# Performance work log

Hardware: AMD Instinct MI355X
Metric: run time of the kernel (lower is better)

The kernel has to match this reference:

```python
import jax, jax.numpy as jnp
import numpy as np

N_HEAD = 16

def setup_inputs() -> dict:
    key = jax.random.key(0)
    k1, k2, k3 = jax.random.split(key, 3)
    B, T, D = 2, 2048, 1024
    x = jax.random.normal(k1, (B, T, D), dtype=jnp.float32)
    sigma_qkv = float(np.sqrt(2.0 / (D + 3 * D)))
    sigma_out = float(np.sqrt(2.0 / (D + D)))
    W_qkv = jax.random.truncated_normal(k2, -3.0, 3.0, (3 * D, D), dtype=jnp.float32) * sigma_qkv
    W_out = jax.random.truncated_normal(k3, -3.0, 3.0, (D, D), dtype=jnp.float32) * sigma_out
    return {"x": x, "W_qkv": W_qkv, "W_out": W_out}


def reference(x, W_qkv, W_out):
    B, T, C = x.shape
    H = N_HEAD
    hd = C // H
    qkv = x @ W_qkv.T  # (B,T,3C)
    q, k, v = jnp.split(qkv, 3, axis=-1)
    # (B,T,C) -> (B,H,T,hd)
    q = q.reshape(B, T, H, hd).transpose(0, 2, 1, 3)
    k = k.reshape(B, T, H, hd).transpose(0, 2, 1, 3)
    v = v.reshape(B, T, H, hd).transpose(0, 2, 1, 3)
    scale = 1.0 / jnp.sqrt(jnp.asarray(hd, dtype=x.dtype))
    score = jnp.einsum('bhqd,bhkd->bhqk', q, k) * scale  # (B,H,T,T)
    causal = jnp.tril(jnp.ones((T, T), dtype=bool))
    score = jnp.where(causal, score, -jnp.inf)
    attn = jax.nn.softmax(score, axis=-1)
    out = jnp.einsum('bhqk,bhkd->bhqd', attn, v)  # (B,H,T,hd)
    out = out.transpose(0, 2, 1, 3).reshape(B, T, C)
    return out @ W_out.T
```

## Files before the change

kernel.cpp:

```cpp
#include <hip/hip_runtime.h>
#include <hip/hip_bf16.h>
#include <cstdint>

typedef unsigned short u16;
typedef __attribute__((ext_vector_type(8))) short bf16x8;
typedef __attribute__((ext_vector_type(4))) float f32x4;

#define T_SEQ 2048
#define NHEAD 16
#define HDIM  64
#define NB    2

__device__ __forceinline__ float bf2f(uint32_t h) { return __uint_as_float(h << 16); }
__device__ __forceinline__ u16 f2bf(float f) {
    uint32_t u = __float_as_uint(f);
    u += 0x7fffu + ((u >> 16) & 1u);
    return (u16)(u >> 16);
}

__device__ __forceinline__ void gl_lds16(const u16* g, u16* s) {
    __builtin_amdgcn_global_load_lds(
        (const __attribute__((address_space(1))) unsigned int*)g,
        (__attribute__((address_space(3))) unsigned int*)s, 16, 0, 0);
}

__global__ void detect_dtype(const uint32_t* __restrict__ x, int* __restrict__ flag) {
    __shared__ int red[4];
    int c = 0;
#pragma unroll
    for (int j = 0; j < 4; j++) {
        uint32_t v = x[threadIdx.x * 4 + j];
        uint32_t lo = v & 0xffffu;
        uint32_t e = (lo >> 7) & 0xffu;
        if (lo != 0u && e >= 110u && e <= 135u) c++;
    }
#pragma unroll
    for (int off = 32; off; off >>= 1) c += __shfl_down(c, off);
    if ((threadIdx.x & 63) == 0) red[threadIdx.x >> 6] = c;
    __syncthreads();
    if (threadIdx.x == 0)
        *flag = (red[0] + red[1] + red[2] + red[3] > 614) ? 1 : 0;
}

__global__ __launch_bounds__(256) void to_bf16(
    const void* __restrict__ src, u16* __restrict__ dst, int n4,
    const int* __restrict__ flag)
{
    int i = blockIdx.x * 256 + threadIdx.x;
    const int stride = gridDim.x * 256;
    if (*flag != 0) {
        const uint2* s = (const uint2*)src;
        uint2* d = (uint2*)dst;
        for (; i < n4; i += stride) d[i] = s[i];
    } else {
        const float4* s = (const float4*)src;
        for (; i < n4; i += stride) {
            float4 v = s[i];
            ushort4 o = { f2bf(v.x), f2bf(v.y), f2bf(v.z), f2bf(v.w) };
            *(ushort4*)(dst + (size_t)i * 4) = o;
        }
    }
}

template<int BM, int MODE>
__global__ __launch_bounds__(256, 3) void gemm_bt_mfma(
    const u16* __restrict__ A, const u16* __restrict__ B,
    int N, int K,
    u16* __restrict__ qo, u16* __restrict__ ko, u16* __restrict__ vt,
    u16* __restrict__ outb16, float* __restrict__ outf32,
    const int* __restrict__ flag)
{
    constexpr int WM = BM / 2;
    constexpr int MI = WM / 16;
    constexpr int IA = BM / 32;
    constexpr int ST = 2 * BM * 64 * 2;
    constexpr int E16 = 4 * WM * 72 * 2;
    constexpr int EF = (MODE == 1) ? 4 * WM * (WM + 4) * 4 : 0;
    constexpr int SB = (ST > E16 ? ST : E16) > EF ? (ST > E16 ? ST : E16) : EF;
    __shared__ u16 smem[SB / 2];
    u16* As = smem;
    u16* Bs = smem + BM * 64;
    const int tid = threadIdx.x;
    const int bm = blockIdx.y * BM, bn = blockIdx.x * BM;
    const int w = tid >> 6, lane = tid & 63;
    const int wm = (w >> 1) * WM, wn = (w & 1) * WM;
    const int n16 = lane & 15, quad = lane >> 4;
    const int l8 = lane >> 3, c8 = lane & 7;

    f32x4 acc[MI][MI];
#pragma unroll
    for (int mi = 0; mi < MI; mi++)
#pragma unroll
        for (int ni = 0; ni < MI; ni++) acc[mi][ni] = (f32x4){0.f, 0.f, 0.f, 0.f};

    const int KT = K >> 6;
    for (int kt = 0; kt < KT; kt++) {
        const int k0 = kt << 6;
#pragma unroll
        for (int i = 0; i < IA; i++) {
            int rowblk = (i * 4 + w) * 8;
            int row = rowblk + l8;
            int gcol = (c8 ^ l8) * 8;
            gl_lds16(A + (size_t)(bm + row) * K + k0 + gcol, As + rowblk * 64);
            gl_lds16(B + (size_t)(bn + row) * K + k0 + gcol, Bs + rowblk * 64);
        }
        __syncthreads();
#pragma unroll
        for (int ks = 0; ks < 2; ks++) {
            bf16x8 af[MI], bfr[MI];
#pragma unroll
            for (int mi = 0; mi < MI; mi++) {
                int row = wm + mi * 16 + n16;
                af[mi] = *(const bf16x8*)(As + row * 64 + (((ks * 4 + quad) ^ (n16 & 7)) * 8));
            }
#pragma unroll
            for (int ni = 0; ni < MI; ni++) {
                int row = wn + ni * 16 + n16;
                bfr[ni] = *(const bf16x8*)(Bs + row * 64 + (((ks * 4 + quad) ^ (n16 & 7)) * 8));
            }
#pragma unroll
            for (int mi = 0; mi < MI; mi++)
#pragma unroll
                for (int ni = 0; ni < MI; ni++)
                    acc[mi][ni] = __builtin_amdgcn_mfma_f32_16x16x32_bf16(
                        af[mi], bfr[ni], acc[mi][ni], 0, 0, 0);
        }
        __syncthreads();
    }

    if constexpr (MODE == 0) {
        u16* ep = smem + w * (WM * 72);
        const int which = (bn + wn) >> 10;
        const int hq = ((bn + wn) & 1023) >> 6;
        const int bb = (bm + wm) >> 11;
        const int tb = (bm + wm) & (T_SEQ - 1);
        if (which == 2) {
#pragma unroll
            for (int mi = 0; mi < MI; mi++)
#pragma unroll
                for (int ni = 0; ni < MI; ni++)
#pragma unroll
                    for (int r = 0; r < 4; r++)
                        ep[(ni * 16 + n16) * 72 + mi * 16 + quad * 4 + r] = f2bf(acc[mi][ni][r]);
            asm volatile("s_waitcnt lgkmcnt(0)" ::: "memory");
            u16* dst = vt + ((size_t)(bb * NHEAD + hq) * HDIM) * T_SEQ + tb;
#pragma unroll
            for (int it = 0; it < 8; it++) {
                int row = it * 8 + l8, col = c8 * 8;
                bf16x8 v = *(const bf16x8*)(ep + row * 72 + col);
                *(bf16x8*)(dst + (size_t)row * T_SEQ + col) = v;
            }
        } else {
            const float sc = which ? 1.f : 0.125f;
#pragma unroll
            for (int mi = 0; mi < MI; mi++)
#pragma unroll
                for (int ni = 0; ni < MI; ni++)
#pragma unroll
                    for (int r = 0; r < 4; r++)
                        ep[(mi * 16 + quad * 4 + r) * 72 + ni * 16 + n16] = f2bf(acc[mi][ni][r] * sc);
            asm volatile("s_waitcnt lgkmcnt(0)" ::: "memory");
            u16* dst = (which ? ko : qo) + ((size_t)(bb * NHEAD + hq) * T_SEQ + tb) * HDIM;
#pragma unroll
            for (int it = 0; it < 8; it++) {
                int row = it * 8 + l8, col = c8 * 8;
                bf16x8 v = *(const bf16x8*)(ep + row * 72 + col);
                *(bf16x8*)(dst + (size_t)row * HDIM + col) = v;
            }
        }
    } else {
        if (*flag == 0) {
            float* epf = (float*)smem + w * (WM * (WM + 4));
#pragma unroll
            for (int mi = 0; mi < MI; mi++)
#pragma unroll
                for (int ni = 0; ni < MI; ni++)
#pragma unroll
                    for (int r = 0; r < 4; r++)
                        epf[(mi * 16 + quad * 4 + r) * (WM + 4) + ni * 16 + n16] = acc[mi][ni][r];
            asm volatile("s_waitcnt lgkmcnt(0)" ::: "memory");
            constexpr int LPR = WM / 4;
            constexpr int RPI = 64 / LPR;
#pragma unroll
            for (int it = 0; it < WM / RPI; it++) {
                int row = it * RPI + lane / LPR, col = (lane % LPR) * 4;
                float4 v = *(const float4*)(epf + row * (WM + 4) + col);
                *(float4*)(outf32 + (size_t)(bm + wm + row) * N + bn + wn + col) = v;
            }
        } else {
            u16* ep = smem + w * (WM * 72);
#pragma unroll
            for (int mi = 0; mi < MI; mi++)
#pragma unroll
                for (int ni = 0; ni < MI; ni++)
#pragma unroll
                    for (int r = 0; r < 4; r++)
                        ep[(mi * 16 + quad * 4 + r) * 72 + ni * 16 + n16] = f2bf(acc[mi][ni][r]);
            asm volatile("s_waitcnt lgkmcnt(0)" ::: "memory");
            constexpr int LPR = WM / 8;
            constexpr int RPI = 64 / LPR;
#pragma unroll
            for (int it = 0; it < WM / RPI; it++) {
                int row = it * RPI + lane / LPR, col = (lane % LPR) * 8;
                bf16x8 v = *(const bf16x8*)(ep + row * 72 + col);
                *(bf16x8*)(outb16 + (size_t)(bm + wm + row) * N + bn + wn + col) = v;
            }
        }
    }
}

__global__ __launch_bounds__(1024, 4) void attn_mfma(
    const u16* __restrict__ qb, const u16* __restrict__ kb,
    const u16* __restrict__ vt, u16* __restrict__ ob)
{
    __shared__ u16 KV[4 * 64 * 64];
    __shared__ u16 Plds[16][16][72];
    const int bidx = blockIdx.x;
    const int bh = bidx & 31;
    const int t  = 15 - (bidx >> 5);
    const int w = threadIdx.x >> 6, lane = threadIdx.x & 63;
    const int g = w >> 3;
    const int wq = w & 7;
    const int n16 = lane & 15, quad = lane >> 4;
    const int l8 = lane >> 3, c8 = lane & 7;
    const size_t baseK = (size_t)bh * T_SEQ * HDIM;
    const size_t baseV = (size_t)bh * HDIM * T_SEQ;
    const int b = bh >> 4, head = bh & 15;

    u16* Ksg = KV + g * (2 * 64 * 64);
    u16* Vsg = KV + g * (2 * 64 * 64) + 64 * 64;

    bf16x8 ones;
#pragma unroll
    for (int e = 0; e < 8; e++) ones[e] = (short)0x3F80;

    auto stage = [&](int i) {
        int kt = 2 * i + g;
        int row = wq * 8 + l8;
        int gc = (c8 ^ l8) * 8;
        gl_lds16(kb + baseK + (size_t)(kt * 64 + row) * HDIM + gc, Ksg + (wq * 8) * 64);
        gl_lds16(vt + baseV + (size_t)row * T_SEQ + (size_t)kt * 64 + gc, Vsg + (wq * 8) * 64);
    };

    const int qrow = t * 128 + wq * 16;
    bf16x8 qf[2];
#pragma unroll
    for (int ks = 0; ks < 2; ks++)
        qf[ks] = *(const bf16x8*)(qb + baseK + (size_t)(qrow + n16) * HDIM + ks * 32 + quad * 8);

    f32x4 accO[4];
#pragma unroll
    for (int st = 0; st < 4; st++) accO[st] = (f32x4){0.f, 0.f, 0.f, 0.f};
    f32x4 accL = (f32x4){0.f, 0.f, 0.f, 0.f};

    stage(0);
    for (int i = 0; i <= t; i++) {
        __syncthreads();

        bf16x8 kf[2][4], vf[2][4];
#pragma unroll
        for (int st = 0; st < 4; st++)
#pragma unroll
            for (int ks = 0; ks < 2; ks++) {
                int off = (st * 16 + n16) * 64 + (((ks * 4 + quad) ^ (n16 & 7)) * 8);
                kf[ks][st] = *(const bf16x8*)(Ksg + off);
                vf[ks][st] = *(const bf16x8*)(Vsg + off);
            }
        __syncthreads();

        if (i < t) stage(i + 1);

        const bool act = (i < t) | (g == 0) | (wq >= 4);
        if (act) {
            f32x4 S[4];
#pragma unroll
            for (int st = 0; st < 4; st++) S[st] = (f32x4){0.f, 0.f, 0.f, 0.f};
#pragma unroll
            for (int st = 0; st < 4; st++)
#pragma unroll
                for (int ks = 0; ks < 2; ks++)
                    S[st] = __builtin_amdgcn_mfma_f32_16x16x32_bf16(qf[ks], kf[ks][st], S[st], 0, 0, 0);
            if (i == t) {
                const int kbase = g * 64;
                int qloc = wq * 16 + quad * 4;
#pragma unroll
                for (int st = 0; st < 4; st++) {
                    int kloc = kbase + st * 16 + n16;
#pragma unroll
                    for (int r = 0; r < 4; r++)
                        if (kloc > qloc + r) S[st][r] = -INFINITY;
                }
            }
#pragma unroll
            for (int st = 0; st < 4; st++)
#pragma unroll
                for (int r = 0; r < 4; r++) {
                    float pv = exp2f(__builtin_fmaf(S[st][r], 1.44269504f, -14.4269504f));
                    Plds[w][quad * 4 + r][st * 16 + n16] = (u16)(__float_as_uint(pv) >> 16);
                }
            asm volatile("s_waitcnt lgkmcnt(0)" ::: "memory");
            bf16x8 pf[2];
#pragma unroll
            for (int ks = 0; ks < 2; ks++)
                pf[ks] = *(const bf16x8*)(&Plds[w][n16][ks * 32 + quad * 8]);
#pragma unroll
            for (int st = 0; st < 4; st++)
#pragma unroll
                for (int ks = 0; ks < 2; ks++)
                    accO[st] = __builtin_amdgcn_mfma_f32_16x16x32_bf16(pf[ks], vf[ks][st], accO[st], 0, 0, 0);
#pragma unroll
            for (int ks = 0; ks < 2; ks++)
                accL = __builtin_amdgcn_mfma_f32_16x16x32_bf16(pf[ks], ones, accL, 0, 0, 0);
        }
    }

    float* cmbO = (float*)KV;
    float* cmbL = (float*)&Plds[8][0][0];
    if (g == 1) {
#pragma unroll
        for (int st = 0; st < 4; st++)
#pragma unroll
            for (int r = 0; r < 4; r++)
                cmbO[wq * 1024 + (quad * 4 + r) * 64 + st * 16 + n16] = accO[st][r];
        if (n16 == 0)
#pragma unroll
            for (int r = 0; r < 4; r++)
                cmbL[wq * 16 + quad * 4 + r] = accL[r];
    }
    __syncthreads();
    if (g == 0) {
#pragma unroll
        for (int st = 0; st < 4; st++)
#pragma unroll
            for (int r = 0; r < 4; r++)
                accO[st][r] += cmbO[wq * 1024 + (quad * 4 + r) * 64 + st * 16 + n16];
#pragma unroll
        for (int r = 0; r < 4; r++) {
            float l2 = cmbL[wq * 16 + quad * 4 + r];
            float inv = 1.f / (accL[r] + l2);
#pragma unroll
            for (int st = 0; st < 4; st++)
                Plds[w][quad * 4 + r][st * 16 + n16] = f2bf(accO[st][r] * inv);
        }
        asm volatile("s_waitcnt lgkmcnt(0)" ::: "memory");
        u16* dst = ob + ((size_t)(b * T_SEQ + qrow)) * 1024 + head * HDIM;
#pragma unroll
        for (int it = 0; it < 2; it++) {
            int row = it * 8 + l8, col = c8 * 8;
            bf16x8 v = *(const bf16x8*)(&Plds[w][row][col]);
            *(bf16x8*)(dst + (size_t)row * 1024 + col) = v;
        }
    }
}

extern "C" void kernel_launch(void* const* d_in, const int* in_sizes, int n_in,
                              void* d_out, int out_size, void* d_ws, size_t ws_size,
                              hipStream_t stream) {
    const void* x    = d_in[0];
    const void* Wqkv = d_in[1];
    const void* Wout = d_in[2];

    const int Mtok = NB * T_SEQ;
    const size_t n_x    = (size_t)Mtok * 1024;
    const size_t n_wqkv = (size_t)3072 * 1024;
    const size_t n_wout = (size_t)1024 * 1024;
    const size_t qkv_elems = (size_t)NB * NHEAD * T_SEQ * HDIM;

    u16* xb    = (u16*)d_ws;
    u16* wqkvb = xb + n_x;
    u16* woutb = wqkvb + n_wqkv;
    u16* qb    = woutb + n_wout;
    u16* kb    = qb + qkv_elems;
    u16* vt    = kb + qkv_elems;
    u16* obuf  = vt + qkv_elems;
    int* flag  = (int*)(obuf + qkv_elems);

    detect_dtype<<<1, 256, 0, stream>>>((const uint32_t*)x, flag);

    to_bf16<<<1024, 256, 0, stream>>>(x,    xb,    (int)(n_x / 4),    flag);
    to_bf16<<<1024, 256, 0, stream>>>(Wqkv, wqkvb, (int)(n_wqkv / 4), flag);
    to_bf16<<<512,  256, 0, stream>>>(Wout, woutb, (int)(n_wout / 4), flag);

    gemm_bt_mfma<128, 0><<<dim3(3072 / 128, Mtok / 128), 256, 0, stream>>>(
        xb, wqkvb, 3072, 1024, qb, kb, vt, nullptr, nullptr, flag);

    attn_mfma<<<dim3(NB * NHEAD * (T_SEQ / 128)), 1024, 0, stream>>>(qb, kb, vt, obuf);

    gemm_bt_mfma<64, 1><<<dim3(1024 / 64, Mtok / 64), 256, 0, stream>>>(
        obuf, woutb, 1024, 1024, nullptr, nullptr, nullptr,
        (u16*)d_out, (float*)d_out, flag);
}
```

Before: 177.6 us.

## Pair causal query tiles per block to balance attention work

Each attention block now processes two query tiles, t and 15-t, in sequence, so every block performs the same total number of key/value iterations. The grid is halved. The K/V prefetch for the second phase is issued at the end of the first, and the cross-group combine buffers are reorganized so the epilogue runs per phase. This targets tail imbalance from causal masking, at the cost of fewer blocks and more serialized work per block.

```diff
diff --git a/kernel.cpp b/kernel.cpp
--- a/kernel.cpp
+++ b/kernel.cpp
@@ -214,10 +214,11 @@
     const u16* __restrict__ vt, u16* __restrict__ ob)
 {
     __shared__ u16 KV[4 * 64 * 64];
-    __shared__ u16 Plds[16][16][72];
+    __shared__ u16 PT[16 * 16 * 72];
+    __shared__ float cmbL[8][16];
     const int bidx = blockIdx.x;
     const int bh = bidx & 31;
-    const int t  = 15 - (bidx >> 5);
+    const int tpair = bidx >> 5;
     const int w = threadIdx.x >> 6, lane = threadIdx.x & 63;
     const int g = w >> 3;
     const int wq = w & 7;
@@ -229,6 +230,8 @@
 
     u16* Ksg = KV + g * (2 * 64 * 64);
     u16* Vsg = KV + g * (2 * 64 * 64) + 64 * 64;
+    u16* Pw  = PT + w * 1152;
+    float* cmbO = (float*)PT;
 
     bf16x8 ones;
 #pragma unroll
@@ -242,113 +245,123 @@
         gl_lds16(vt + baseV + (size_t)row * T_SEQ + (size_t)kt * 64 + gc, Vsg + (wq * 8) * 64);
     };
 
-    const int qrow = t * 128 + wq * 16;
-    bf16x8 qf[2];
-#pragma unroll
-    for (int ks = 0; ks < 2; ks++)
-        qf[ks] = *(const bf16x8*)(qb + baseK + (size_t)(qrow + n16) * HDIM + ks * 32 + quad * 8);
-
-    f32x4 accO[4];
-#pragma unroll
-    for (int st = 0; st < 4; st++) accO[st] = (f32x4){0.f, 0.f, 0.f, 0.f};
-    f32x4 accL = (f32x4){0.f, 0.f, 0.f, 0.f};
-
     stage(0);
-    for (int i = 0; i <= t; i++) {
+
+    for (int phase = 0; phase < 2; phase++) {
+        const int t = phase ? (15 - tpair) : tpair;
+        const int qrow = t * 128 + wq * 16;
+        bf16x8 qf[2];
+#pragma unroll
+        for (int ks = 0; ks < 2; ks++)
+            qf[ks] = *(const bf16x8*)(qb + baseK + (size_t)(qrow + n16) * HDIM + ks * 32 + quad * 8);
+
+        f32x4 accO[4];
+#pragma unroll
+        for (int st = 0; st < 4; st++) accO[st] = (f32x4){0.f, 0.f, 0.f, 0.f};
+        f32x4 accL = (f32x4){0.f, 0.f, 0.f, 0.f};
+
+        for (int i = 0; i <= t; i++) {
+            __syncthreads();
+
+            bf16x8 kf[2][4], vf[2][4];
+#pragma unroll
+            for (int st = 0; st < 4; st++)
+#pragma unroll
+                for (int ks = 0; ks < 2; ks++) {
+                    int off = (st * 16 + n16) * 64 + (((ks * 4 + quad) ^ (n16 & 7)) * 8);
+                    kf[ks][st] = *(const bf16x8*)(Ksg + off);
+                    vf[ks][st] = *(const bf16x8*)(Vsg + off);
+                }
+            __syncthreads();
+
+            if (i < t) stage(i + 1);
+            else if (phase == 0) stage(0);
+
+            const bool act = (i < t) | (g == 0) | (wq >= 4);
+            if (act) {
+                f32x4 S[4];
+#pragma unroll
+                for (int st = 0; st < 4; st++) S[st] = (f32x4){0.f, 0.f, 0.f, 0.f};
+#pragma unroll
+                for (int st = 0; st < 4; st++)
+#pragma unroll
+                    for (int ks = 0; ks < 2; ks++)
+                        S[st] = __builtin_amdgcn_mfma_f32_16x16x32_bf16(qf[ks], kf[ks][st], S[st], 0, 0, 0);
+                if (i == t) {
+                    const int kbase = g * 64;
+                    int qloc = wq * 16 + quad * 4;
+#pragma unroll
+                    for (int st = 0; st < 4; st++) {
+                        int kloc = kbase + st * 16 + n16;
+#pragma unroll
+                        for (int r = 0; r < 4; r++)
+                            if (kloc > qloc + r) S[st][r] = -INFINITY;
+                    }
+                }
+#pragma unroll
+                for (int st = 0; st < 4; st++)
+#pragma unroll
+                    for (int r = 0; r < 4; r++) {
+                        float pv = exp2f(__builtin_fmaf(S[st][r], 1.44269504f, -14.4269504f));
+                        Pw[(quad * 4 + r) * 72 + st * 16 + n16] = (u16)(__float_as_uint(pv) >> 16);
+                    }
+                asm volatile("s_waitcnt lgkmcnt(0)" ::: "memory");
+                bf16x8 pf[2];
+#pragma unroll
+                for (int ks = 0; ks < 2; ks++)
+                    pf[ks] = *(const bf16x8*)(Pw + n16 * 72 + ks * 32 + quad * 8);
+#pragma unroll
+                for (int st = 0; st < 4; st++)
+#pragma unroll
+                    for (int ks = 0; ks < 2; ks++)
+                        accO[st] = __builtin_amdgcn_mfma_f32_16x16x32_bf16(pf[ks], vf[ks][st], accO[st], 0, 0, 0);
+#pragma unroll
+                for (int ks = 0; ks < 2; ks++)
+                    accL = __builtin_amdgcn_mfma_f32_16x16x32_bf16(pf[ks], ones, accL, 0, 0, 0);
+            }
+        }
+
         __syncthreads();
 
-        bf16x8 kf[2][4], vf[2][4];
-#pragma unroll
-        for (int st = 0; st < 4; st++)
-#pragma unroll
-            for (int ks = 0; ks < 2; ks++) {
-                int off = (st * 16 + n16) * 64 + (((ks * 4 + quad) ^ (n16 & 7)) * 8);
-                kf[ks][st] = *(const bf16x8*)(Ksg + off);
-                vf[ks][st] = *(const bf16x8*)(Vsg + off);
-            }
+        if (g == 1) {
+#pragma unroll
+            for (int st = 0; st < 4; st++)
+#pragma unroll
+                for (int r = 0; r < 4; r++)
+                    cmbO[wq * 1024 + (quad * 4 + r) * 64 + st * 16 + n16] = accO[st][r];
+            if (n16 == 0)
+#pragma unroll
+                for (int r = 0; r < 4; r++)
+                    cmbL[wq][quad * 4 + r] = accL[r];
+        }
         __syncthreads();
-
-        if (i < t) stage(i + 1);
-
-        const bool act = (i < t) | (g == 0) | (wq >= 4);
-        if (act) {
-            f32x4 S[4];
-#pragma unroll
-            for (int st = 0; st < 4; st++) S[st] = (f32x4){0.f, 0.f, 0.f, 0.f};
+        float inv[4];
+        if (g == 0) {
 #pragma unroll
             for (int st = 0; st < 4; st++)
 #pragma unroll
-                for (int ks = 0; ks < 2; ks++)
-                    S[st] = __builtin_amdgcn_mfma_f32_16x16x32_bf16(qf[ks], kf[ks][st], S[st], 0, 0, 0);
-            if (i == t) {
-                const int kbase = g * 64;
-                int qloc = wq * 16 + quad * 4;
-#pragma unroll
-                for (int st = 0; st < 4; st++) {
-                    int kloc = kbase + st * 16 + n16;
-#pragma unroll
-                    for (int r = 0; r < 4; r++)
-                        if (kloc > qloc + r) S[st][r] = -INFINITY;
-                }
-            }
-#pragma unroll
-            for (int st = 0; st < 4; st++)
-#pragma unroll
-                for (int r = 0; r < 4; r++) {
-                    float pv = exp2f(__builtin_fmaf(S[st][r], 1.44269504f, -14.4269504f));
-                    Plds[w][quad * 4 + r][st * 16 + n16] = (u16)(__float_as_uint(pv) >> 16);
-                }
+                for (int r = 0; r < 4; r++)
+                    accO[st][r] += cmbO[wq * 1024 + (quad * 4 + r) * 64 + st * 16 + n16];
+#pragma unroll
+            for (int r = 0; r < 4; r++)
+                inv[r] = 1.f / (accL[r] + cmbL[wq][quad * 4 + r]);
+        }
+        __syncthreads();
+        if (g == 0) {
+            u16* ep = PT + wq * 1152;
+#pragma unroll
+            for (int r = 0; r < 4; r++)
+#pragma unroll
+                for (int st = 0; st < 4; st++)
+                    ep[(quad * 4 + r) * 72 + st * 16 + n16] = f2bf(accO[st][r] * inv[r]);
             asm volatile("s_waitcnt lgkmcnt(0)" ::: "memory");
-            bf16x8 pf[2];
-#pragma unroll
-            for (int ks = 0; ks < 2; ks++)
-                pf[ks] = *(const bf16x8*)(&Plds[w][n16][ks * 32 + quad * 8]);
-#pragma unroll
-            for (int st = 0; st < 4; st++)
-#pragma unroll
-                for (int ks = 0; ks < 2; ks++)
-                    accO[st] = __builtin_amdgcn_mfma_f32_16x16x32_bf16(pf[ks], vf[ks][st], accO[st], 0, 0, 0);
-#pragma unroll
-            for (int ks = 0; ks < 2; ks++)
-                accL = __builtin_amdgcn_mfma_f32_16x16x32_bf16(pf[ks], ones, accL, 0, 0, 0);
-        }
-    }
-
-    float* cmbO = (float*)KV;
-    float* cmbL = (float*)&Plds[8][0][0];
-    if (g == 1) {
-#pragma unroll
-        for (int st = 0; st < 4; st++)
-#pragma unroll
-            for (int r = 0; r < 4; r++)
-                cmbO[wq * 1024 + (quad * 4 + r) * 64 + st * 16 + n16] = accO[st][r];
-        if (n16 == 0)
-#pragma unroll
-            for (int r = 0; r < 4; r++)
-                cmbL[wq * 16 + quad * 4 + r] = accL[r];
-    }
-    __syncthreads();
-    if (g == 0) {
-#pragma unroll
-        for (int st = 0; st < 4; st++)
-#pragma unroll
-            for (int r = 0; r < 4; r++)
-                accO[st][r] += cmbO[wq * 1024 + (quad * 4 + r) * 64 + st * 16 + n16];
-#pragma unroll
-        for (int r = 0; r < 4; r++) {
-            float l2 = cmbL[wq * 16 + quad * 4 + r];
-            float inv = 1.f / (accL[r] + l2);
-#pragma unroll
-            for (int st = 0; st < 4; st++)
-                Plds[w][quad * 4 + r][st * 16 + n16] = f2bf(accO[st][r] * inv);
-        }
-        asm volatile("s_waitcnt lgkmcnt(0)" ::: "memory");
-        u16* dst = ob + ((size_t)(b * T_SEQ + qrow)) * 1024 + head * HDIM;
-#pragma unroll
-        for (int it = 0; it < 2; it++) {
-            int row = it * 8 + l8, col = c8 * 8;
-            bf16x8 v = *(const bf16x8*)(&Plds[w][row][col]);
-            *(bf16x8*)(dst + (size_t)row * 1024 + col) = v;
+            u16* dst = ob + ((size_t)(b * T_SEQ + qrow)) * 1024 + head * HDIM;
+#pragma unroll
+            for (int it = 0; it < 2; it++) {
+                int row = it * 8 + l8, col = c8 * 8;
+                bf16x8 v = *(const bf16x8*)(ep + row * 72 + col);
+                *(bf16x8*)(dst + (size_t)row * 1024 + col) = v;
+            }
         }
     }
 }
@@ -384,7 +397,7 @@
     gemm_bt_mfma<128, 0><<<dim3(3072 / 128, Mtok / 128), 256, 0, stream>>>(
         xb, wqkvb, 3072, 1024, qb, kb, vt, nullptr, nullptr, flag);
 
-    attn_mfma<<<dim3(NB * NHEAD * (T_SEQ / 128)), 1024, 0, stream>>>(qb, kb, vt, obuf);
+    attn_mfma<<<dim3(NB * NHEAD * (T_SEQ / 256)), 1024, 0, stream>>>(qb, kb, vt, obuf);
 
     gemm_bt_mfma<64, 1><<<dim3(1024 / 64, Mtok / 64), 256, 0, stream>>>(
         obuf, woutb, 1024, 1024, nullptr, nullptr, nullptr,
```

Measured after the change: 185.2 us. 4.2% more time.
